# Kernel optimization log

Measured on AMD Instinct MI355X. Metric: run time of the kernel, lower is better.

## Reference

```python
import jax, jax.numpy as jnp
import numpy as np


def setup_inputs() -> dict:
    key = jax.random.key(0)
    ks = jax.random.split(key, 8)
    B, N, F = 16, 2048, 128
    x = jax.random.normal(ks[0], (B, N, F), dtype=jnp.float32)
    # dense (pre-normalized) adjacency, as spektral GCNConv expects normalized A
    a = jax.random.uniform(ks[1], (B, N, N), dtype=jnp.float32) / N
    w1 = jax.random.normal(ks[2], (F, 32), dtype=jnp.float32) * 0.1
    b1 = jnp.zeros((32,), dtype=jnp.float32)
    w2 = jax.random.normal(ks[3], (32, 32), dtype=jnp.float32) * 0.1
    b2 = jnp.zeros((32,), dtype=jnp.float32)
    wf1 = jax.random.normal(ks[4], (32, 512), dtype=jnp.float32) * 0.1
    bf1 = jnp.zeros((512,), dtype=jnp.float32)
    wf2 = jax.random.normal(ks[5], (512, 1), dtype=jnp.float32) * 0.1
    bf2 = jnp.zeros((1,), dtype=jnp.float32)
    return {"x": x, "a": a, "w1": w1, "b1": b1, "w2": w2, "b2": b2,
            "wf1": wf1, "bf1": bf1, "wf2": wf2, "bf2": bf2}


def _gcn(x, a, w, b):
    # GCNConv: elu(A_norm @ X @ W + b)
    h = jnp.einsum('bnf,fc->bnc', x, w)   # dense transform first (cheaper)
    h = jnp.einsum('bnm,bmc->bnc', a, h)  # adjacency aggregation
    return jax.nn.elu(h + b)


def reference(x, a, w1, b1, w2, b2, wf1, bf1, wf2, bf2):
    h = _gcn(x, a, w1, b1)                # [B,N,32]
    h = _gcn(h, a, w2, b2)                # [B,N,32]
    pooled = jnp.sum(h, axis=1)           # GlobalSumPool -> [B,32]
    h = jax.nn.relu(pooled @ wf1 + bf1)   # [B,512]
    out = jax.nn.sigmoid(h @ wf2 + bf2)   # [B,1]
    return out
```

## Files before the change

### kernel.cpp

```cpp
#include <hip/hip_runtime.h>
#include <hip/hip_bf16.h>
#include <math.h>

#define BATCH 16
#define NN 2048
#define FF 128
#define CC 32
#define HID 512
#define QM 512
#define LSTR 520

typedef float v4f __attribute__((ext_vector_type(4)));
typedef float v2f __attribute__((ext_vector_type(2)));
typedef short short8 __attribute__((ext_vector_type(8)));

__device__ __forceinline__ unsigned short f2bf(float f) {
  unsigned u = __float_as_uint(f);
  u += 0x7fffu + ((u >> 16) & 1u);
  return (unsigned short)(u >> 16);
}

__device__ __forceinline__ float elu1(float x) {
  return x > 0.f ? x : expm1f(x);
}

__global__ __launch_bounds__(256)
void k_xw1(const float* __restrict__ src, const float* __restrict__ w,
           unsigned short* __restrict__ outT) {
  int t = threadIdx.x;
  int wv = t >> 6, l = t & 63, lo = l & 15, q = l >> 4;
  int rowt = blockIdx.x * 4 + wv;
  long row = (long)rowt * 16 + lo;

  short8 wf[FF / 32][2];
#pragma unroll
  for (int kc = 0; kc < FF / 32; ++kc)
#pragma unroll
    for (int h = 0; h < 2; ++h) {
      short8 f;
#pragma unroll
      for (int j = 0; j < 8; ++j)
        f[j] = (short)f2bf(w[(kc * 32 + q * 8 + j) * CC + h * 16 + lo]);
      wf[kc][h] = f;
    }

  v4f acc0 = {0.f, 0.f, 0.f, 0.f}, acc1 = {0.f, 0.f, 0.f, 0.f};
#pragma unroll
  for (int kc = 0; kc < FF / 32; ++kc) {
    const float* sp = src + row * FF + kc * 32 + q * 8;
    float4 a0 = *(const float4*)sp;
    float4 a1 = *(const float4*)(sp + 4);
    short8 af;
    af[0] = (short)f2bf(a0.x); af[1] = (short)f2bf(a0.y);
    af[2] = (short)f2bf(a0.z); af[3] = (short)f2bf(a0.w);
    af[4] = (short)f2bf(a1.x); af[5] = (short)f2bf(a1.y);
    af[6] = (short)f2bf(a1.z); af[7] = (short)f2bf(a1.w);
    acc0 = __builtin_amdgcn_mfma_f32_16x16x32_bf16(af, wf[kc][0], acc0, 0, 0, 0);
    acc1 = __builtin_amdgcn_mfma_f32_16x16x32_bf16(af, wf[kc][1], acc1, 0, 0, 0);
  }

  int b = rowt >> 7;
  int nbase = (rowt & 127) * 16;
#pragma unroll
  for (int r = 0; r < 4; ++r) {
    int n = nbase + q * 4 + r;
    outT[((long)b * CC + lo) * NN + n] = f2bf(acc0[r]);
    outT[((long)b * CC + 16 + lo) * NN + n] = f2bf(acc1[r]);
  }
}

__global__ __launch_bounds__(256, 4)
void k_agg1(const float* __restrict__ a, unsigned char* __restrict__ afp8,
            const unsigned short* __restrict__ hT, float* __restrict__ hpart) {
  __shared__ unsigned short hs[CC * LSTR];

  int t = threadIdx.x;
  int bid = blockIdx.x;
  int rt = bid & 31, qm = (bid >> 5) & 3, b = bid >> 7;

#pragma unroll
  for (int i = 0; i < 8; ++i) {
    int j = i * 256 + t;
    int c = j >> 6, off = (j & 63) * 8;
    *(uint4*)&hs[c * LSTR + off] =
        *(const uint4*)(hT + ((long)b * CC + c) * NN + qm * QM + off);
  }
  __syncthreads();

  int wv = t >> 6, l = t & 63, lo = l & 15, q = l >> 4;
  int n0 = rt * 64 + wv * 16;
  long abase = ((long)(b * NN + n0 + lo)) * NN + qm * QM + q * 8;
  const float* arow = a + abase;
  unsigned char* aout = afp8 + abase;
  const unsigned short* h0 = &hs[lo * LSTR + q * 8];

  v4f acc0 = {0.f, 0.f, 0.f, 0.f}, acc1 = {0.f, 0.f, 0.f, 0.f};
#pragma unroll
  for (int mm = 0; mm < QM; mm += 32) {
    float4 a0 = *(const float4*)(arow + mm);
    float4 a1 = *(const float4*)(arow + mm + 4);
    short8 af;
    af[0] = (short)f2bf(a0.x); af[1] = (short)f2bf(a0.y);
    af[2] = (short)f2bf(a0.z); af[3] = (short)f2bf(a0.w);
    af[4] = (short)f2bf(a1.x); af[5] = (short)f2bf(a1.y);
    af[6] = (short)f2bf(a1.z); af[7] = (short)f2bf(a1.w);
    const float sc = 1024.f;
    int w0 = __builtin_amdgcn_cvt_pk_fp8_f32(a0.x * sc, a0.y * sc, 0, false);
    w0 = __builtin_amdgcn_cvt_pk_fp8_f32(a0.z * sc, a0.w * sc, w0, true);
    int w1 = __builtin_amdgcn_cvt_pk_fp8_f32(a1.x * sc, a1.y * sc, 0, false);
    w1 = __builtin_amdgcn_cvt_pk_fp8_f32(a1.z * sc, a1.w * sc, w1, true);
    *(int2*)(aout + mm) = make_int2(w0, w1);
    short8 b0 = *(const short8*)(h0 + mm);
    short8 b1 = *(const short8*)(h0 + 16 * LSTR + mm);
    acc0 = __builtin_amdgcn_mfma_f32_16x16x32_bf16(af, b0, acc0, 0, 0, 0);
    acc1 = __builtin_amdgcn_mfma_f32_16x16x32_bf16(af, b1, acc1, 0, 0, 0);
  }

  float* op = hpart + ((long)qm * BATCH * NN + (long)b * NN) * CC;
#pragma unroll
  for (int r = 0; r < 4; ++r) {
    int n = n0 + q * 4 + r;
    op[(long)n * CC + lo] = acc0[r];
    op[(long)n * CC + 16 + lo] = acc1[r];
  }
}

__global__ __launch_bounds__(256)
void k_xw2(const float* __restrict__ h1p, const float* __restrict__ b1,
           const float* __restrict__ w2, unsigned short* __restrict__ outT) {
  const long QS = (long)BATCH * NN * CC;
  int t = threadIdx.x;
  int wv = t >> 6, l = t & 63, lo = l & 15, q = l >> 4;
  int rowt = blockIdx.x * 4 + wv;
  long row = (long)rowt * 16 + lo;

  short8 wf[2];
#pragma unroll
  for (int h = 0; h < 2; ++h) {
    short8 f;
#pragma unroll
    for (int j = 0; j < 8; ++j)
      f[j] = (short)f2bf(w2[(q * 8 + j) * CC + h * 16 + lo]);
    wf[h] = f;
  }

  const float* p = h1p + row * CC + q * 8;
  float s[8] = {0, 0, 0, 0, 0, 0, 0, 0};
#pragma unroll
  for (int qq = 0; qq < 4; ++qq) {
    float4 u0 = *(const float4*)(p + qq * QS);
    float4 u1 = *(const float4*)(p + qq * QS + 4);
    s[0] += u0.x; s[1] += u0.y; s[2] += u0.z; s[3] += u0.w;
    s[4] += u1.x; s[5] += u1.y; s[6] += u1.z; s[7] += u1.w;
  }
  short8 af;
#pragma unroll
  for (int j = 0; j < 8; ++j)
    af[j] = (short)f2bf(elu1(s[j] + b1[q * 8 + j]));

  v4f acc0 = {0.f, 0.f, 0.f, 0.f}, acc1 = {0.f, 0.f, 0.f, 0.f};
  acc0 = __builtin_amdgcn_mfma_f32_16x16x32_bf16(af, wf[0], acc0, 0, 0, 0);
  acc1 = __builtin_amdgcn_mfma_f32_16x16x32_bf16(af, wf[1], acc1, 0, 0, 0);

  const float inv = 1.f / 1024.f;
  int b = rowt >> 7;
  int nbase = (rowt & 127) * 16;
#pragma unroll
  for (int r = 0; r < 4; ++r) {
    int n = nbase + q * 4 + r;
    outT[((long)b * CC + lo) * NN + n] = f2bf(acc0[r] * inv);
    outT[((long)b * CC + 16 + lo) * NN + n] = f2bf(acc1[r] * inv);
  }
}

__global__ __launch_bounds__(256, 4)
void k_agg2(const unsigned char* __restrict__ afp8,
            const unsigned short* __restrict__ hT, float* __restrict__ hpart) {
  __shared__ unsigned short hs[CC * LSTR];

  int t = threadIdx.x;
  int bid = blockIdx.x;
  int rt = bid & 31, qm = (bid >> 5) & 3, b = bid >> 7;

#pragma unroll
  for (int i = 0; i < 8; ++i) {
    int j = i * 256 + t;
    int c = j >> 6, off = (j & 63) * 8;
    *(uint4*)&hs[c * LSTR + off] =
        *(const uint4*)(hT + ((long)b * CC + c) * NN + qm * QM + off);
  }
  __syncthreads();

  int wv = t >> 6, l = t & 63, lo = l & 15, q = l >> 4;
  int n0 = rt * 64 + wv * 16;
  const unsigned char* arow =
      afp8 + ((long)(b * NN + n0 + lo)) * NN + qm * QM + q * 8;
  const unsigned short* h0 = &hs[lo * LSTR + q * 8];

  v4f acc0 = {0.f, 0.f, 0.f, 0.f}, acc1 = {0.f, 0.f, 0.f, 0.f};
#pragma unroll
  for (int mm = 0; mm < QM; mm += 32) {
    int2 av = *(const int2*)(arow + mm);
    v2f f01 = __builtin_amdgcn_cvt_pk_f32_fp8(av.x, false);
    v2f f23 = __builtin_amdgcn_cvt_pk_f32_fp8(av.x, true);
    v2f f45 = __builtin_amdgcn_cvt_pk_f32_fp8(av.y, false);
    v2f f67 = __builtin_amdgcn_cvt_pk_f32_fp8(av.y, true);
    short8 af;
    af[0] = (short)f2bf(f01.x); af[1] = (short)f2bf(f01.y);
    af[2] = (short)f2bf(f23.x); af[3] = (short)f2bf(f23.y);
    af[4] = (short)f2bf(f45.x); af[5] = (short)f2bf(f45.y);
    af[6] = (short)f2bf(f67.x); af[7] = (short)f2bf(f67.y);
    short8 b0 = *(const short8*)(h0 + mm);
    short8 b1 = *(const short8*)(h0 + 16 * LSTR + mm);
    acc0 = __builtin_amdgcn_mfma_f32_16x16x32_bf16(af, b0, acc0, 0, 0, 0);
    acc1 = __builtin_amdgcn_mfma_f32_16x16x32_bf16(af, b1, acc1, 0, 0, 0);
  }

  float* op = hpart + ((long)qm * BATCH * NN + (long)b * NN) * CC;
#pragma unroll
  for (int r = 0; r < 4; ++r) {
    int n = n0 + q * 4 + r;
    op[(long)n * CC + lo] = acc0[r];
    op[(long)n * CC + 16 + lo] = acc1[r];
  }
}

__global__ __launch_bounds__(256)
void k_pool(const float* __restrict__ h2p, const float* __restrict__ b2,
            float* __restrict__ pp) {
  const long QS = (long)BATCH * NN * CC;
  __shared__ float red[8][CC + 1];
  int t = threadIdx.x;
  int b = blockIdx.x >> 3, seg = blockIdx.x & 7;
  int c = t & 31, nl = t >> 5;
  float bc = b2[c];
  float s = 0.f;
  for (int n = seg * 256 + nl; n < seg * 256 + 256; n += 8) {
    long idx = ((long)b * NN + n) * CC + c;
    s += elu1(h2p[idx] + h2p[QS + idx] + h2p[2 * QS + idx] + h2p[3 * QS + idx] + bc);
  }
  red[nl][c] = s;
  __syncthreads();
  if (nl < 4) red[nl][c] += red[nl + 4][c];
  __syncthreads();
  if (nl < 2) red[nl][c] += red[nl + 2][c];
  __syncthreads();
  if (nl == 0) pp[((long)seg * BATCH + b) * CC + c] = red[0][c] + red[1][c];
}

__global__ __launch_bounds__(512)
void k5_mlp(const float* __restrict__ pp, const float* __restrict__ wf1,
            const float* __restrict__ bf1, const float* __restrict__ wf2,
            const float* __restrict__ bf2, float* __restrict__ out) {
  __shared__ float red[HID];
  __shared__ float ps[CC];
  int b = blockIdx.x, j = threadIdx.x;
  if (j < CC) {
    float s = 0.f;
#pragma unroll
    for (int g = 0; g < 8; ++g) s += pp[((long)g * BATCH + b) * CC + j];
    ps[j] = s;
  }
  __syncthreads();
  float acc = bf1[j];
#pragma unroll
  for (int c = 0; c < CC; ++c) acc += ps[c] * wf1[c * HID + j];
  red[j] = fmaxf(acc, 0.f) * wf2[j];
  __syncthreads();
  for (int s = HID / 2; s > 0; s >>= 1) {
    if (j < s) red[j] += red[j + s];
    __syncthreads();
  }
  if (j == 0) out[b] = 1.f / (1.f + expf(-(red[0] + bf2[0])));
}

extern "C" void kernel_launch(void* const* d_in, const int* in_sizes, int n_in,
                              void* d_out, int out_size, void* d_ws, size_t ws_size,
                              hipStream_t stream) {
  const float* x   = (const float*)d_in[0];
  const float* a   = (const float*)d_in[1];
  const float* w1  = (const float*)d_in[2];
  const float* b1  = (const float*)d_in[3];
  const float* w2  = (const float*)d_in[4];
  const float* b2  = (const float*)d_in[5];
  const float* wf1 = (const float*)d_in[6];
  const float* bf1 = (const float*)d_in[7];
  const float* wf2 = (const float*)d_in[8];
  const float* bf2 = (const float*)d_in[9];
  float* out = (float*)d_out;

  char* ws = (char*)d_ws;
  unsigned char*  afp8 = (unsigned char*)ws;
  unsigned short* hT1  = (unsigned short*)(ws + 0x4000000UL);
  unsigned short* hT2  = (unsigned short*)(ws + 0x4200000UL);
  float* h1p = (float*)(ws + 0x4400000UL);
  float* h2p = (float*)(ws + 0x5400000UL);
  float* pp  = (float*)(ws + 0x6400000UL);

  k_xw1<<<512, 256, 0, stream>>>(x, w1, hT1);
  k_agg1<<<2048, 256, 0, stream>>>(a, afp8, hT1, h1p);
  k_xw2<<<512, 256, 0, stream>>>(h1p, b1, w2, hT2);
  k_agg2<<<2048, 256, 0, stream>>>(afp8, hT2, h2p);
  k_pool<<<128, 256, 0, stream>>>(h2p, b2, pp);
  k5_mlp<<<BATCH, HID, 0, stream>>>(pp, wf1, bf1, wf2, bf2, out);
}
```

Before: 447.5 us.

## Stage adjacency tiles through swizzled LDS with coalesced loads in aggregation kernels

Both aggregation kernels now load adjacency rows cooperatively, with each row read contiguously by 32 threads, and stage them in XOR-swizzled shared memory. Before, each lane read strided 32-byte fragments directly from global memory. k_agg1 double-buffers 128-column bf16 tiles and prefetches the next slice into registers while MFMAs consume the current one. k_agg2 stages the whole fp8 slab in LDS up front. The larger LDS footprint lowers the occupancy hint from 4 to 2 blocks per CU, which may reduce latency hiding.

```diff
diff --git a/kernel.cpp b/kernel.cpp
--- a/kernel.cpp
+++ b/kernel.cpp
@@ -9,10 +9,12 @@
 #define HID 512
 #define QM 512
 #define LSTR 520
+#define KS1 128
 
 typedef float v4f __attribute__((ext_vector_type(4)));
 typedef float v2f __attribute__((ext_vector_type(2)));
 typedef short short8 __attribute__((ext_vector_type(8)));
+typedef short s4v __attribute__((ext_vector_type(4)));
 
 __device__ __forceinline__ unsigned short f2bf(float f) {
   unsigned u = __float_as_uint(f);
@@ -69,57 +71,94 @@
   }
 }
 
-__global__ __launch_bounds__(256, 4)
+__global__ __launch_bounds__(256, 2)
 void k_agg1(const float* __restrict__ a, unsigned char* __restrict__ afp8,
             const unsigned short* __restrict__ hT, float* __restrict__ hpart) {
-  __shared__ unsigned short hs[CC * LSTR];
+  __shared__ __attribute__((aligned(16))) unsigned short hs[CC * LSTR];
+  __shared__ __attribute__((aligned(16))) unsigned short at[2][64 * KS1];
 
   int t = threadIdx.x;
   int bid = blockIdx.x;
   int rt = bid & 31, qm = (bid >> 5) & 3, b = bid >> 7;
+  int n0 = rt * 64;
+
+  int r0 = t >> 5, chunk = t & 31;
+  const float* ga = a + ((long)(b * NN + n0 + r0)) * NN + qm * QM + chunk * 4;
+  unsigned char* gao = afp8 + ((long)(b * NN + n0 + r0)) * NN + qm * QM + chunk * 4;
+  int swb = r0 * 256 + ((chunk * 8) ^ (r0 << 4));
+
+  float4 ar[8];
+  const float sc = 1024.f;
+
+#pragma unroll
+  for (int j = 0; j < 8; ++j)
+    ar[j] = *(const float4*)(ga + (long)j * 8 * NN);
 
 #pragma unroll
   for (int i = 0; i < 8; ++i) {
-    int j = i * 256 + t;
-    int c = j >> 6, off = (j & 63) * 8;
+    int jj = i * 256 + t;
+    int c = jj >> 6, off = (jj & 63) * 8;
     *(uint4*)&hs[c * LSTR + off] =
         *(const uint4*)(hT + ((long)b * CC + c) * NN + qm * QM + off);
   }
-  __syncthreads();
-
-  int wv = t >> 6, l = t & 63, lo = l & 15, q = l >> 4;
-  int n0 = rt * 64 + wv * 16;
-  long abase = ((long)(b * NN + n0 + lo)) * NN + qm * QM + q * 8;
-  const float* arow = a + abase;
-  unsigned char* aout = afp8 + abase;
+
+#pragma unroll
+  for (int j = 0; j < 8; ++j) {
+    char* lp = (char*)&at[0][0] + swb + j * 2048;
+    s4v bv;
+    bv[0] = (short)f2bf(ar[j].x); bv[1] = (short)f2bf(ar[j].y);
+    bv[2] = (short)f2bf(ar[j].z); bv[3] = (short)f2bf(ar[j].w);
+    *(s4v*)lp = bv;
+    int w0 = __builtin_amdgcn_cvt_pk_fp8_f32(ar[j].x * sc, ar[j].y * sc, 0, false);
+    w0 = __builtin_amdgcn_cvt_pk_fp8_f32(ar[j].z * sc, ar[j].w * sc, w0, true);
+    *(int*)(gao + (long)j * 8 * NN) = w0;
+  }
+  __syncthreads();
+
+  int l = t & 63, wv = t >> 6, lo = l & 15, q = l >> 4;
+  int lrow = wv * 16 + lo;
   const unsigned short* h0 = &hs[lo * LSTR + q * 8];
 
   v4f acc0 = {0.f, 0.f, 0.f, 0.f}, acc1 = {0.f, 0.f, 0.f, 0.f};
-#pragma unroll
-  for (int mm = 0; mm < QM; mm += 32) {
-    float4 a0 = *(const float4*)(arow + mm);
-    float4 a1 = *(const float4*)(arow + mm + 4);
-    short8 af;
-    af[0] = (short)f2bf(a0.x); af[1] = (short)f2bf(a0.y);
-    af[2] = (short)f2bf(a0.z); af[3] = (short)f2bf(a0.w);
-    af[4] = (short)f2bf(a1.x); af[5] = (short)f2bf(a1.y);
-    af[6] = (short)f2bf(a1.z); af[7] = (short)f2bf(a1.w);
-    const float sc = 1024.f;
-    int w0 = __builtin_amdgcn_cvt_pk_fp8_f32(a0.x * sc, a0.y * sc, 0, false);
-    w0 = __builtin_amdgcn_cvt_pk_fp8_f32(a0.z * sc, a0.w * sc, w0, true);
-    int w1 = __builtin_amdgcn_cvt_pk_fp8_f32(a1.x * sc, a1.y * sc, 0, false);
-    w1 = __builtin_amdgcn_cvt_pk_fp8_f32(a1.z * sc, a1.w * sc, w1, true);
-    *(int2*)(aout + mm) = make_int2(w0, w1);
-    short8 b0 = *(const short8*)(h0 + mm);
-    short8 b1 = *(const short8*)(h0 + 16 * LSTR + mm);
-    acc0 = __builtin_amdgcn_mfma_f32_16x16x32_bf16(af, b0, acc0, 0, 0, 0);
-    acc1 = __builtin_amdgcn_mfma_f32_16x16x32_bf16(af, b1, acc1, 0, 0, 0);
+
+#pragma unroll
+  for (int ks = 0; ks < 4; ++ks) {
+    if (ks < 3) {
+#pragma unroll
+      for (int j = 0; j < 8; ++j)
+        ar[j] = *(const float4*)(ga + (long)j * 8 * NN + (ks + 1) * KS1);
+    }
+    const char* ab = (const char*)at + (ks & 1) * (64 * KS1 * 2);
+#pragma unroll
+    for (int kk = 0; kk < 4; ++kk) {
+      short8 af = *(const short8*)(ab + lrow * 256 + ((q * 16 + kk * 64) ^ ((lo & 7) << 4)));
+      int m = ks * KS1 + kk * 32;
+      short8 b0 = *(const short8*)(h0 + m);
+      short8 b1 = *(const short8*)(h0 + 16 * LSTR + m);
+      acc0 = __builtin_amdgcn_mfma_f32_16x16x32_bf16(af, b0, acc0, 0, 0, 0);
+      acc1 = __builtin_amdgcn_mfma_f32_16x16x32_bf16(af, b1, acc1, 0, 0, 0);
+    }
+    if (ks < 3) {
+      char* lb = (char*)&at[(ks + 1) & 1][0];
+#pragma unroll
+      for (int j = 0; j < 8; ++j) {
+        char* lp = lb + swb + j * 2048;
+        s4v bv;
+        bv[0] = (short)f2bf(ar[j].x); bv[1] = (short)f2bf(ar[j].y);
+        bv[2] = (short)f2bf(ar[j].z); bv[3] = (short)f2bf(ar[j].w);
+        *(s4v*)lp = bv;
+        int w0 = __builtin_amdgcn_cvt_pk_fp8_f32(ar[j].x * sc, ar[j].y * sc, 0, false);
+        w0 = __builtin_amdgcn_cvt_pk_fp8_f32(ar[j].z * sc, ar[j].w * sc, w0, true);
+        *(int*)(gao + (long)j * 8 * NN + (ks + 1) * KS1) = w0;
+      }
+      __syncthreads();
+    }
   }
 
   float* op = hpart + ((long)qm * BATCH * NN + (long)b * NN) * CC;
 #pragma unroll
   for (int r = 0; r < 4; ++r) {
-    int n = n0 + q * 4 + r;
+    int n = n0 + wv * 16 + q * 4 + r;
     op[(long)n * CC + lo] = acc0[r];
     op[(long)n * CC + 16 + lo] = acc1[r];
   }
@@ -173,34 +212,49 @@
   }
 }
 
-__global__ __launch_bounds__(256, 4)
+__global__ __launch_bounds__(256, 2)
 void k_agg2(const unsigned char* __restrict__ afp8,
             const unsigned short* __restrict__ hT, float* __restrict__ hpart) {
-  __shared__ unsigned short hs[CC * LSTR];
+  __shared__ __attribute__((aligned(16))) unsigned short hs[CC * LSTR];
+  __shared__ __attribute__((aligned(16))) unsigned char a2[64 * QM];
 
   int t = threadIdx.x;
   int bid = blockIdx.x;
   int rt = bid & 31, qm = (bid >> 5) & 3, b = bid >> 7;
+  int n0 = rt * 64;
+
+  int r0 = t >> 5, chunk = t & 31;
+  const unsigned char* ga =
+      afp8 + ((long)(b * NN + n0 + r0)) * NN + qm * QM + chunk * 16;
+  char* lw = (char*)a2 + r0 * 512 + ((chunk * 16) ^ (r0 << 4));
+
+  uint4 arr[8];
+#pragma unroll
+  for (int j = 0; j < 8; ++j)
+    arr[j] = *(const uint4*)(ga + (long)j * 8 * NN);
 
 #pragma unroll
   for (int i = 0; i < 8; ++i) {
-    int j = i * 256 + t;
-    int c = j >> 6, off = (j & 63) * 8;
+    int jj = i * 256 + t;
+    int c = jj >> 6, off = (jj & 63) * 8;
     *(uint4*)&hs[c * LSTR + off] =
         *(const uint4*)(hT + ((long)b * CC + c) * NN + qm * QM + off);
   }
-  __syncthreads();
-
-  int wv = t >> 6, l = t & 63, lo = l & 15, q = l >> 4;
-  int n0 = rt * 64 + wv * 16;
-  const unsigned char* arow =
-      afp8 + ((long)(b * NN + n0 + lo)) * NN + qm * QM + q * 8;
+
+#pragma unroll
+  for (int j = 0; j < 8; ++j)
+    *(uint4*)(lw + j * 4096) = arr[j];
+  __syncthreads();
+
+  int l = t & 63, wv = t >> 6, lo = l & 15, q = l >> 4;
+  int lrow = wv * 16 + lo;
   const unsigned short* h0 = &hs[lo * LSTR + q * 8];
+  const char* ab = (const char*)a2;
 
   v4f acc0 = {0.f, 0.f, 0.f, 0.f}, acc1 = {0.f, 0.f, 0.f, 0.f};
 #pragma unroll
-  for (int mm = 0; mm < QM; mm += 32) {
-    int2 av = *(const int2*)(arow + mm);
+  for (int kk = 0; kk < 16; ++kk) {
+    int2 av = *(const int2*)(ab + lrow * 512 + ((q * 8 + kk * 32) ^ ((lo & 7) << 4)));
     v2f f01 = __builtin_amdgcn_cvt_pk_f32_fp8(av.x, false);
     v2f f23 = __builtin_amdgcn_cvt_pk_f32_fp8(av.x, true);
     v2f f45 = __builtin_amdgcn_cvt_pk_f32_fp8(av.y, false);
@@ -210,8 +264,9 @@
     af[2] = (short)f2bf(f23.x); af[3] = (short)f2bf(f23.y);
     af[4] = (short)f2bf(f45.x); af[5] = (short)f2bf(f45.y);
     af[6] = (short)f2bf(f67.x); af[7] = (short)f2bf(f67.y);
-    short8 b0 = *(const short8*)(h0 + mm);
-    short8 b1 = *(const short8*)(h0 + 16 * LSTR + mm);
+    int m = kk * 32;
+    short8 b0 = *(const short8*)(h0 + m);
+    short8 b1 = *(const short8*)(h0 + 16 * LSTR + m);
     acc0 = __builtin_amdgcn_mfma_f32_16x16x32_bf16(af, b0, acc0, 0, 0, 0);
     acc1 = __builtin_amdgcn_mfma_f32_16x16x32_bf16(af, b1, acc1, 0, 0, 0);
   }
@@ -219,7 +274,7 @@
   float* op = hpart + ((long)qm * BATCH * NN + (long)b * NN) * CC;
 #pragma unroll
   for (int r = 0; r < 4; ++r) {
-    int n = n0 + q * 4 + r;
+    int n = n0 + wv * 16 + q * 4 + r;
     op[(long)n * CC + lo] = acc0[r];
     op[(long)n * CC + 16 + lo] = acc1[r];
   }
```

New measurement: 431.5 us, median of 2. 3.6% less time.
